# Kernel optimization log

Measured on AMD Instinct MI355X. Metric: run time of the kernel, lower is better.

Reference implementation:

```python
import jax, jax.numpy as jnp
import numpy as np

GRID_SIZE = 5
K = 3  # spline order
WIDTH = [512, 1024, 1024, 1024, 256]
BATCH = 4096


def make_grid(in_dim):
    # pykan-style extended uniform grid on [-1, 1]: G + 2K + 1 knots per input dim
    h = 2.0 / GRID_SIZE
    pts = jnp.arange(-K, GRID_SIZE + K + 1, dtype=jnp.float32) * h - 1.0
    return jnp.tile(pts[None, :], (in_dim, 1))


def bspline_basis(x, grid):
    # Cox-de Boor recursion. x: [B, in], grid: [in, G+2K+1] -> basis [B, in, G+K]
    xe = x[..., None]
    b = ((xe >= grid[:, :-1]) & (xe < grid[:, 1:])).astype(x.dtype)  # degree 0: [B, in, G+2K]
    for d in range(1, K + 1):
        left = (xe - grid[:, :-(d + 1)]) / (grid[:, d:-1] - grid[:, :-(d + 1)]) * b[..., :-1]
        right = (grid[:, d + 1:] - xe) / (grid[:, d + 1:] - grid[:, 1:-d]) * b[..., 1:]
        b = left + right
    return b


def kan_layer(x, grid, coef, scale_base, scale_sp):
    # out_j = sum_i scale_base[i,j]*silu(x_i) + scale_sp[i,j]*sum_g coef[i,j,g]*B_g(x_i)
    basis = bspline_basis(x, grid)                                   # [B, in, G+K]
    base = jnp.einsum('bi,io->bo', jax.nn.silu(x), scale_base)
    spline = jnp.einsum('big,iog->bo', basis, coef * scale_sp[:, :, None])
    return base + spline


def setup_inputs() -> dict:
    key = jax.random.key(0)
    n_layers = len(WIDTH) - 1
    keys = jax.random.split(key, 2 + 2 * n_layers)
    inp = {
        'inputs_y': jax.random.normal(keys[0], (BATCH, 256), dtype=jnp.float32) * 0.5,
        'inputs_u': jax.random.normal(keys[1], (BATCH, 256), dtype=jnp.float32) * 0.5,
    }
    for l, (din, dout) in enumerate(zip(WIDTH[:-1], WIDTH[1:])):
        inp[f'coef{l}'] = jax.random.normal(keys[2 + 2 * l], (din, dout, GRID_SIZE + K), dtype=jnp.float32) * (0.1 / np.sqrt(din))
        inp[f'sb{l}'] = jax.random.normal(keys[3 + 2 * l], (din, dout), dtype=jnp.float32) * (1.0 / np.sqrt(din))
        inp[f'ss{l}'] = jnp.ones((din, dout), dtype=jnp.float32)
        inp[f'grid{l}'] = make_grid(din)
    return inp


def reference(inputs_y, inputs_u,
              coef0, sb0, ss0, grid0,
              coef1, sb1, ss1, grid1,
              coef2, sb2, ss2, grid2,
              coef3, sb3, ss3, grid3):
    x = jnp.concatenate([inputs_y.astype(jnp.float32), inputs_u.astype(jnp.float32)], axis=-1)
    layers = [(grid0, coef0, sb0, ss0), (grid1, coef1, sb1, ss1),
              (grid2, coef2, sb2, ss2), (grid3, coef3, sb3, ss3)]
    for g, c, sb, ss in layers:
        x = kan_layer(x, g, c, sb, ss)
    return x
```

## Files before the change

kernel.cpp:

```cpp
#include <hip/hip_runtime.h>
#include <cstdint>
#include <cstddef>

typedef _Float16 f16;
typedef _Float16 f16x4 __attribute__((ext_vector_type(4)));
typedef _Float16 f16x8 __attribute__((ext_vector_type(8)));
typedef float f32x4 __attribute__((ext_vector_type(4)));

__device__ __forceinline__ void gl2lds16(const void* g, void* l) {
  __builtin_amdgcn_global_load_lds(
      (const __attribute__((address_space(1))) void*)(uintptr_t)g,
      (__attribute__((address_space(3))) void*)(uintptr_t)l,
      16, 0, 0);
}

__global__ __launch_bounds__(256) void kan_prep2(
    const float* __restrict__ coef, const float* __restrict__ sb,
    const float* __restrict__ ss, f16* __restrict__ Wt,
    int out, int K9)
{
  __shared__ float s_sb[32][32];
  __shared__ float s_ss[32][32];
  __shared__ f16 s_w[32][288];
  const int t  = threadIdx.x;
  const int o0 = blockIdx.x * 32, i0 = blockIdx.y * 32;

  {
    int il = t >> 3, oc = (t & 7) * 4;
    float4 vb = *(const float4*)(sb + (size_t)(i0 + il) * out + o0 + oc);
    float4 vs = *(const float4*)(ss + (size_t)(i0 + il) * out + o0 + oc);
    s_sb[il][oc + 0] = vb.x; s_sb[il][oc + 1] = vb.y;
    s_sb[il][oc + 2] = vb.z; s_sb[il][oc + 3] = vb.w;
    s_ss[il][oc + 0] = vs.x; s_ss[il][oc + 1] = vs.y;
    s_ss[il][oc + 2] = vs.z; s_ss[il][oc + 3] = vs.w;
  }
  __syncthreads();

#pragma unroll
  for (int j = 0; j < 8; ++j) {
    int f  = j * 256 + t;
    int il = f >> 6, c = f & 63;
    int ol = c >> 1, gh = (c & 1) * 4;
    float4 v = *(const float4*)(coef + ((size_t)(i0 + il) * out + (o0 + ol)) * 8 + gh);
    float ssv = s_ss[il][ol];
    f16* dst = &s_w[ol][il * 9 + 1 + gh];
    dst[0] = (f16)(v.x * ssv); dst[1] = (f16)(v.y * ssv);
    dst[2] = (f16)(v.z * ssv); dst[3] = (f16)(v.w * ssv);
  }
#pragma unroll
  for (int j = 0; j < 4; ++j) {
    int e = j * 256 + t; int il = e >> 5, ol = e & 31;
    s_w[ol][il * 9] = (f16)s_sb[il][ol];
  }
  __syncthreads();

  {
    int o = t >> 3, part = t & 7;
    f16* dst = Wt + (size_t)(o0 + o) * K9 + (size_t)i0 * 9 + part * 36;
    const f16* src = &s_w[o][part * 36];
#pragma unroll
    for (int q = 0; q < 9; ++q)
      *(f16x4*)(dst + q * 4) = *(const f16x4*)(src + q * 4);
  }
}

__global__ __launch_bounds__(256) void kan_feat(
    const float* __restrict__ X, f16* __restrict__ F,
    int shift, int K9, int iBase)
{
  int idx = blockIdx.x * 256 + threadIdx.x;
  int b  = idx >> shift;
  int ii = idx & ((1 << shift) - 1);
  float x = X[idx];

  float sig  = 1.0f / (1.0f + __expf(-x));
  float silu = x * sig;

  float t[12];
#pragma unroll
  for (int j = 0; j < 12; ++j) t[j] = (float)(j - 3) * 0.4f - 1.0f;
  float b0[11];
#pragma unroll
  for (int j = 0; j < 11; ++j)
    b0[j] = (x >= t[j] && x < t[j + 1]) ? 1.0f : 0.0f;
  float b1[10];
#pragma unroll
  for (int j = 0; j < 10; ++j)
    b1[j] = (x - t[j]) * 2.5f * b0[j] + (t[j + 2] - x) * 2.5f * b0[j + 1];
  float b2[9];
#pragma unroll
  for (int j = 0; j < 9; ++j)
    b2[j] = (x - t[j]) * 1.25f * b1[j] + (t[j + 3] - x) * 1.25f * b1[j + 1];
  float b3[8];
#pragma unroll
  for (int j = 0; j < 8; ++j)
    b3[j] = (x - t[j]) * (1.0f / 1.2f) * b2[j] +
            (t[j + 4] - x) * (1.0f / 1.2f) * b2[j + 1];

  f16* o = F + (size_t)b * K9 + (size_t)(iBase + ii) * 9;
  o[0] = (f16)silu;
#pragma unroll
  for (int g = 0; g < 8; ++g) o[1 + g] = (f16)b3[g];
}

template <int SPLITK>
__global__ __launch_bounds__(256, 2) void kan_gemm(
    const f16* __restrict__ A, const f16* __restrict__ Bt,
    float* __restrict__ C, int N, int K)
{
  __shared__ __align__(16) f16 lds[4][8192];
  const int tid   = threadIdx.x;
  const int lane  = tid & 63;
  const int w     = tid >> 6;
  const int waveM = w >> 1, waveN = w & 1;
  const int l16   = lane & 15, quad = lane >> 4;
  const size_t mBase = (size_t)blockIdx.y * 128;
  const size_t nBase = (size_t)blockIdx.x * 128;
  const int kChunk = K / SPLITK;
  const int k0     = blockIdx.z * kChunk;
  const int kSteps = kChunk >> 5;

  const f16* gA[2]; int lA[2];
  const f16* gB[2]; int lB[2];
#pragma unroll
  for (int r = 0; r < 2; ++r) {
    int g = r * 256 + tid, row = g >> 2;
    int cs = (g & 3) ^ ((row >> 1) & 3);
    gA[r] = A + (mBase + row) * (size_t)K + k0 + cs * 8;
    gB[r] = Bt + (nBase + row) * (size_t)K + k0 + cs * 8;
    lA[r] = (r * 256 + (tid & ~63)) * 8;
    lB[r] = 4096 + lA[r];
  }

  f32x4 acc[4][4] = {};

#pragma unroll
  for (int p = 0; p < 3; ++p) {
    f16* b = lds[p];
    int kk = p * 32;
#pragma unroll
    for (int r = 0; r < 2; ++r) {
      gl2lds16(gA[r] + kk, b + lA[r]);
      gl2lds16(gB[r] + kk, b + lB[r]);
    }
  }

  for (int s = 0; s < kSteps; ++s) {
    if (s < kSteps - 2)       asm volatile("s_waitcnt vmcnt(8)" ::: "memory");
    else if (s == kSteps - 2) asm volatile("s_waitcnt vmcnt(4)" ::: "memory");
    else                      asm volatile("s_waitcnt vmcnt(0)" ::: "memory");
    __builtin_amdgcn_s_barrier();

    if (s + 3 < kSteps) {
      int kk = (s + 3) * 32;
      f16* b = lds[(s + 3) & 3];
#pragma unroll
      for (int r = 0; r < 2; ++r) {
        gl2lds16(gA[r] + kk, b + lA[r]);
        gl2lds16(gB[r] + kk, b + lB[r]);
      }
    }

    const f16* buf = lds[s & 3];
    f16x8 af[4], bf[4];
#pragma unroll
    for (int mi = 0; mi < 4; ++mi) {
      int row = waveM * 64 + mi * 16 + l16;
      af[mi] = *(const f16x8*)(buf + row * 32 + (quad ^ ((row >> 1) & 3)) * 8);
    }
#pragma unroll
    for (int ni = 0; ni < 4; ++ni) {
      int col = waveN * 64 + ni * 16 + l16;
      bf[ni] = *(const f16x8*)(buf + 4096 + col * 32 + (quad ^ ((col >> 1) & 3)) * 8);
    }
#pragma unroll
    for (int mi = 0; mi < 4; ++mi)
#pragma unroll
      for (int ni = 0; ni < 4; ++ni)
        acc[mi][ni] = __builtin_amdgcn_mfma_f32_16x16x32_f16(
            af[mi], bf[ni], acc[mi][ni], 0, 0, 0);
  }

#pragma unroll
  for (int mi = 0; mi < 4; ++mi) {
    size_t row = mBase + waveM * 64 + mi * 16 + quad * 4;
#pragma unroll
    for (int ni = 0; ni < 4; ++ni) {
      size_t col = nBase + waveN * 64 + ni * 16 + l16;
#pragma unroll
      for (int r = 0; r < 4; ++r)
        unsafeAtomicAdd(C + (row + r) * N + col, acc[mi][ni][r]);
    }
  }
}

extern "C" void kernel_launch(void* const* d_in, const int* in_sizes, int n_in,
                              void* d_out, int out_size, void* d_ws, size_t ws_size,
                              hipStream_t stream)
{
  const float* y = (const float*)d_in[0];
  const float* u = (const float*)d_in[1];
  const float* coef[4]; const float* sb[4]; const float* ss[4];
  for (int l = 0; l < 4; ++l) {
    coef[l] = (const float*)d_in[2 + 4 * l];
    sb[l]   = (const float*)d_in[3 + 4 * l];
    ss[l]   = (const float*)d_in[4 + 4 * l];
  }
  char* ws = (char*)d_ws;
  f16*   Wt   = (f16*)(ws);
  f16*   F    = (f16*)(ws + 18874368);
  float* actA = (float*)(ws + 18874368 + 75497472);
  float* actB = (float*)(ws + 18874368 + 75497472 + 16777216);
  float* out  = (float*)d_out;
  const size_t actBytes = (size_t)4096 * 1024 * 4;

  kan_prep2<<<dim3(32, 16), 256, 0, stream>>>(coef[0], sb[0], ss[0], Wt, 1024, 4608);
  kan_feat<<<4096 * 256 / 256, 256, 0, stream>>>(y, F, 8, 4608, 0);
  kan_feat<<<4096 * 256 / 256, 256, 0, stream>>>(u, F, 8, 4608, 256);
  hipMemsetAsync(actA, 0, actBytes, stream);
  kan_gemm<2><<<dim3(8, 32, 2), 256, 0, stream>>>(F, Wt, actA, 1024, 4608);

  kan_prep2<<<dim3(32, 32), 256, 0, stream>>>(coef[1], sb[1], ss[1], Wt, 1024, 9216);
  kan_feat<<<4096 * 1024 / 256, 256, 0, stream>>>(actA, F, 10, 9216, 0);
  hipMemsetAsync(actB, 0, actBytes, stream);
  kan_gemm<2><<<dim3(8, 32, 2), 256, 0, stream>>>(F, Wt, actB, 1024, 9216);

  kan_prep2<<<dim3(32, 32), 256, 0, stream>>>(coef[2], sb[2], ss[2], Wt, 1024, 9216);
  kan_feat<<<4096 * 1024 / 256, 256, 0, stream>>>(actB, F, 10, 9216, 0);
  hipMemsetAsync(actA, 0, actBytes, stream);
  kan_gemm<2><<<dim3(8, 32, 2), 256, 0, stream>>>(F, Wt, actA, 1024, 9216);

  kan_prep2<<<dim3(8, 32), 256, 0, stream>>>(coef[3], sb[3], ss[3], Wt, 256, 9216);
  kan_feat<<<4096 * 1024 / 256, 256, 0, stream>>>(actA, F, 10, 9216, 0);
  hipMemsetAsync(d_out, 0, (size_t)out_size * sizeof(float), stream);
  kan_gemm<8><<<dim3(2, 32, 8), 256, 0, stream>>>(F, Wt, out, 256, 9216);
}
```

Before: 621.2 us.

## Fuse weight prep and feature kernels, switch K layout to basis-major

Merges the per-layer weight-packing and B-spline feature kernels into one launch, with blocks split by index between the two jobs. The K dimension changes from input-major interleaved (i*9+g) to basis-major (g*din+i), so the feature kernel writes packed f16x2 pairs, each covering two inputs, instead of scattered 2-byte stores. Memsets are batched up front so fewer memset calls sit between layers. The prep side now gathers strided elements from LDS to build its stores, which may add bank conflicts.

```diff
diff --git a/kernel.cpp b/kernel.cpp
--- a/kernel.cpp
+++ b/kernel.cpp
@@ -3,6 +3,7 @@
 #include <cstddef>
 
 typedef _Float16 f16;
+typedef _Float16 f16x2 __attribute__((ext_vector_type(2)));
 typedef _Float16 f16x4 __attribute__((ext_vector_type(4)));
 typedef _Float16 f16x8 __attribute__((ext_vector_type(8)));
 typedef float f32x4 __attribute__((ext_vector_type(4)));
@@ -14,93 +15,113 @@
       16, 0, 0);
 }
 
-__global__ __launch_bounds__(256) void kan_prep2(
+__device__ __forceinline__ void kan_basis(float x, f16* out9) {
+  float sig  = 1.0f / (1.0f + __expf(-x));
+  out9[0] = (f16)(x * sig);
+
+  float t[12];
+#pragma unroll
+  for (int j = 0; j < 12; ++j) t[j] = (float)(j - 3) * 0.4f - 1.0f;
+  float b0[11];
+#pragma unroll
+  for (int j = 0; j < 11; ++j)
+    b0[j] = (x >= t[j] && x < t[j + 1]) ? 1.0f : 0.0f;
+  float b1[10];
+#pragma unroll
+  for (int j = 0; j < 10; ++j)
+    b1[j] = (x - t[j]) * 2.5f * b0[j] + (t[j + 2] - x) * 2.5f * b0[j + 1];
+  float b2[9];
+#pragma unroll
+  for (int j = 0; j < 9; ++j)
+    b2[j] = (x - t[j]) * 1.25f * b1[j] + (t[j + 3] - x) * 1.25f * b1[j + 1];
+#pragma unroll
+  for (int j = 0; j < 8; ++j)
+    out9[1 + j] = (f16)((x - t[j]) * (1.0f / 1.2f) * b2[j] +
+                        (t[j + 4] - x) * (1.0f / 1.2f) * b2[j + 1]);
+}
+
+__global__ __launch_bounds__(256) void kan_prep_feat(
     const float* __restrict__ coef, const float* __restrict__ sb,
     const float* __restrict__ ss, f16* __restrict__ Wt,
-    int out, int K9)
+    const float* __restrict__ Xa, const float* __restrict__ Xb,
+    f16* __restrict__ F,
+    int dout, int din, int prepBlocks, int featB, int segW, int bShift)
 {
   __shared__ float s_sb[32][32];
   __shared__ float s_ss[32][32];
   __shared__ f16 s_w[32][288];
-  const int t  = threadIdx.x;
-  const int o0 = blockIdx.x * 32, i0 = blockIdx.y * 32;
-
-  {
-    int il = t >> 3, oc = (t & 7) * 4;
-    float4 vb = *(const float4*)(sb + (size_t)(i0 + il) * out + o0 + oc);
-    float4 vs = *(const float4*)(ss + (size_t)(i0 + il) * out + o0 + oc);
-    s_sb[il][oc + 0] = vb.x; s_sb[il][oc + 1] = vb.y;
-    s_sb[il][oc + 2] = vb.z; s_sb[il][oc + 3] = vb.w;
-    s_ss[il][oc + 0] = vs.x; s_ss[il][oc + 1] = vs.y;
-    s_ss[il][oc + 2] = vs.z; s_ss[il][oc + 3] = vs.w;
-  }
-  __syncthreads();
-
-#pragma unroll
-  for (int j = 0; j < 8; ++j) {
-    int f  = j * 256 + t;
-    int il = f >> 6, c = f & 63;
-    int ol = c >> 1, gh = (c & 1) * 4;
-    float4 v = *(const float4*)(coef + ((size_t)(i0 + il) * out + (o0 + ol)) * 8 + gh);
-    float ssv = s_ss[il][ol];
-    f16* dst = &s_w[ol][il * 9 + 1 + gh];
-    dst[0] = (f16)(v.x * ssv); dst[1] = (f16)(v.y * ssv);
-    dst[2] = (f16)(v.z * ssv); dst[3] = (f16)(v.w * ssv);
-  }
-#pragma unroll
-  for (int j = 0; j < 4; ++j) {
-    int e = j * 256 + t; int il = e >> 5, ol = e & 31;
-    s_w[ol][il * 9] = (f16)s_sb[il][ol];
-  }
-  __syncthreads();
-
-  {
-    int o = t >> 3, part = t & 7;
-    f16* dst = Wt + (size_t)(o0 + o) * K9 + (size_t)i0 * 9 + part * 36;
-    const f16* src = &s_w[o][part * 36];
-#pragma unroll
-    for (int q = 0; q < 9; ++q)
-      *(f16x4*)(dst + q * 4) = *(const f16x4*)(src + q * 4);
-  }
-}
-
-__global__ __launch_bounds__(256) void kan_feat(
-    const float* __restrict__ X, f16* __restrict__ F,
-    int shift, int K9, int iBase)
-{
-  int idx = blockIdx.x * 256 + threadIdx.x;
-  int b  = idx >> shift;
-  int ii = idx & ((1 << shift) - 1);
-  float x = X[idx];
-
-  float sig  = 1.0f / (1.0f + __expf(-x));
-  float silu = x * sig;
-
-  float t[12];
-#pragma unroll
-  for (int j = 0; j < 12; ++j) t[j] = (float)(j - 3) * 0.4f - 1.0f;
-  float b0[11];
-#pragma unroll
-  for (int j = 0; j < 11; ++j)
-    b0[j] = (x >= t[j] && x < t[j + 1]) ? 1.0f : 0.0f;
-  float b1[10];
-#pragma unroll
-  for (int j = 0; j < 10; ++j)
-    b1[j] = (x - t[j]) * 2.5f * b0[j] + (t[j + 2] - x) * 2.5f * b0[j + 1];
-  float b2[9];
-#pragma unroll
-  for (int j = 0; j < 9; ++j)
-    b2[j] = (x - t[j]) * 1.25f * b1[j] + (t[j + 3] - x) * 1.25f * b1[j + 1];
-  float b3[8];
-#pragma unroll
-  for (int j = 0; j < 8; ++j)
-    b3[j] = (x - t[j]) * (1.0f / 1.2f) * b2[j] +
-            (t[j + 4] - x) * (1.0f / 1.2f) * b2[j + 1];
-
-  f16* o = F + (size_t)b * K9 + (size_t)(iBase + ii) * 9;
-  o[0] = (f16)silu;
-#pragma unroll
-  for (int g = 0; g < 8; ++g) o[1 + g] = (f16)b3[g];
+  const int t = threadIdx.x;
+  const int gid = blockIdx.x;
+  const int K9 = 9 * din;
+
+  if (gid < prepBlocks) {
+    const int prepBX = dout >> 5;
+    const int o0 = (gid % prepBX) * 32, i0 = (gid / prepBX) * 32;
+
+    {
+      int il = t >> 3, oc = (t & 7) * 4;
+      float4 vb = *(const float4*)(sb + (size_t)(i0 + il) * dout + o0 + oc);
+      float4 vs = *(const float4*)(ss + (size_t)(i0 + il) * dout + o0 + oc);
+      s_sb[il][oc + 0] = vb.x; s_sb[il][oc + 1] = vb.y;
+      s_sb[il][oc + 2] = vb.z; s_sb[il][oc + 3] = vb.w;
+      s_ss[il][oc + 0] = vs.x; s_ss[il][oc + 1] = vs.y;
+      s_ss[il][oc + 2] = vs.z; s_ss[il][oc + 3] = vs.w;
+    }
+    __syncthreads();
+
+#pragma unroll
+    for (int j = 0; j < 8; ++j) {
+      int f  = j * 256 + t;
+      int il = f >> 6, c = f & 63;
+      int ol = c >> 1, gh = (c & 1) * 4;
+      float4 v = *(const float4*)(coef + ((size_t)(i0 + il) * dout + (o0 + ol)) * 8 + gh);
+      float ssv = s_ss[il][ol];
+      f16* dst = &s_w[ol][il * 9 + 1 + gh];
+      dst[0] = (f16)(v.x * ssv); dst[1] = (f16)(v.y * ssv);
+      dst[2] = (f16)(v.z * ssv); dst[3] = (f16)(v.w * ssv);
+    }
+#pragma unroll
+    for (int j = 0; j < 4; ++j) {
+      int e = j * 256 + t; int il = e >> 5, ol = e & 31;
+      s_w[ol][il * 9] = (f16)s_sb[il][ol];
+    }
+    __syncthreads();
+
+    {
+      int o = t >> 3, part = t & 7;
+      f16* dstRow = Wt + (size_t)(o0 + o) * K9 + i0 + part * 4;
+#pragma unroll
+      for (int tp = 0; tp < 9; ++tp) {
+        f16x4 v;
+#pragma unroll
+        for (int j = 0; j < 4; ++j) v[j] = s_w[o][(part * 4 + j) * 9 + tp];
+        *(f16x4*)(dstRow + (size_t)tp * din) = v;
+      }
+    }
+    return;
+  }
+
+  int f   = gid - prepBlocks;
+  int seg = (f >= featB) ? 1 : 0;
+  int fi  = f - seg * featB;
+  const float* X = seg ? Xb : Xa;
+  const int halfW = segW >> 1;
+  int idx2 = fi * 256 + t;
+  int b  = idx2 >> bShift;
+  int ii = idx2 & (halfW - 1);
+  int i  = seg * segW + 2 * ii;
+
+  float2 xv = *(const float2*)(X + (size_t)b * segW + 2 * ii);
+  f16 s0[9], s1[9];
+  kan_basis(xv.x, s0);
+  kan_basis(xv.y, s1);
+
+  f16* o = F + (size_t)b * K9 + i;
+#pragma unroll
+  for (int tp = 0; tp < 9; ++tp) {
+    f16x2 v; v[0] = s0[tp]; v[1] = s1[tp];
+    *(f16x2*)(o + (size_t)tp * din) = v;
+  }
 }
 
 template <int SPLITK>
@@ -214,24 +235,24 @@
   float* out  = (float*)d_out;
   const size_t actBytes = (size_t)4096 * 1024 * 4;
 
-  kan_prep2<<<dim3(32, 16), 256, 0, stream>>>(coef[0], sb[0], ss[0], Wt, 1024, 4608);
-  kan_feat<<<4096 * 256 / 256, 256, 0, stream>>>(y, F, 8, 4608, 0);
-  kan_feat<<<4096 * 256 / 256, 256, 0, stream>>>(u, F, 8, 4608, 256);
+  hipMemsetAsync(actA, 0, 2 * actBytes, stream);
+  hipMemsetAsync(d_out, 0, (size_t)out_size * sizeof(float), stream);
+
+  kan_prep_feat<<<512 + 4096, 256, 0, stream>>>(
+      coef[0], sb[0], ss[0], Wt, y, u, F, 1024, 512, 512, 2048, 256, 7);
+  kan_gemm<2><<<dim3(8, 32, 2), 256, 0, stream>>>(F, Wt, actA, 1024, 4608);
+
+  kan_prep_feat<<<1024 + 8192, 256, 0, stream>>>(
+      coef[1], sb[1], ss[1], Wt, actA, nullptr, F, 1024, 1024, 1024, 8192, 1024, 9);
+  kan_gemm<2><<<dim3(8, 32, 2), 256, 0, stream>>>(F, Wt, actB, 1024, 9216);
+
   hipMemsetAsync(actA, 0, actBytes, stream);
-  kan_gemm<2><<<dim3(8, 32, 2), 256, 0, stream>>>(F, Wt, actA, 1024, 4608);
-
-  kan_prep2<<<dim3(32, 32), 256, 0, stream>>>(coef[1], sb[1], ss[1], Wt, 1024, 9216);
-  kan_feat<<<4096 * 1024 / 256, 256, 0, stream>>>(actA, F, 10, 9216, 0);
-  hipMemsetAsync(actB, 0, actBytes, stream);
-  kan_gemm<2><<<dim3(8, 32, 2), 256, 0, stream>>>(F, Wt, actB, 1024, 9216);
-
-  kan_prep2<<<dim3(32, 32), 256, 0, stream>>>(coef[2], sb[2], ss[2], Wt, 1024, 9216);
-  kan_feat<<<4096 * 1024 / 256, 256, 0, stream>>>(actB, F, 10, 9216, 0);
-  hipMemsetAsync(actA, 0, actBytes, stream);
+
+  kan_prep_feat<<<1024 + 8192, 256, 0, stream>>>(
+      coef[2], sb[2], ss[2], Wt, actB, nullptr, F, 1024, 1024, 1024, 8192, 1024, 9);
   kan_gemm<2><<<dim3(8, 32, 2), 256, 0, stream>>>(F, Wt, actA, 1024, 9216);
 
-  kan_prep2<<<dim3(8, 32), 256, 0, stream>>>(coef[3], sb[3], ss[3], Wt, 256, 9216);
-  kan_feat<<<4096 * 1024 / 256, 256, 0, stream>>>(actA, F, 10, 9216, 0);
-  hipMemsetAsync(d_out, 0, (size_t)out_size * sizeof(float), stream);
+  kan_prep_feat<<<256 + 8192, 256, 0, stream>>>(
+      coef[3], sb[3], ss[3], Wt, actA, nullptr, F, 256, 1024, 256, 8192, 1024, 9);
   kan_gemm<8><<<dim3(2, 32, 8), 256, 0, stream>>>(F, Wt, out, 256, 9216);
 }
```

Result: faster. 590.9 us (-4.9%).
